# Performance work log

Measured on AMD Instinct MI355X. Metric: run time of the kernel, lower is better.

The kernel has to match this reference:

```python
import jax, jax.numpy as jnp
import numpy as np

B, N, IN_DIM, OUT_DIM = 8, 2048, 256, 256
EDGE_P = 0.02   # adjacency density
MASK_P = 0.9    # fraction of valid nodes


def setup_inputs() -> dict:
    key = jax.random.key(0)
    ks = jax.random.split(key, 8)
    x = jax.random.normal(ks[0], (B, N, IN_DIM), dtype=jnp.float32)
    adj = (jax.random.uniform(ks[1], (B, N, N)) < EDGE_P).astype(jnp.float32)
    mask = (jax.random.uniform(ks[2], (B, N)) < MASK_P).astype(jnp.float32)
    # nn.Linear(in_dim, out_dim): W [out, in], b [out]
    lim1 = 1.0 / np.sqrt(IN_DIM)
    W = jax.random.uniform(ks[3], (OUT_DIM, IN_DIM), minval=-lim1, maxval=lim1, dtype=jnp.float32)
    b = jax.random.uniform(ks[4], (OUT_DIM,), minval=-lim1, maxval=lim1, dtype=jnp.float32)
    # nn.Linear(2*out_dim, 1): weight [1, 2D] split into a1 (acts on h_i), a2 (acts on h_j)
    lim2 = 1.0 / np.sqrt(2 * OUT_DIM)
    a1 = jax.random.uniform(ks[5], (OUT_DIM,), minval=-lim2, maxval=lim2, dtype=jnp.float32)
    a2 = jax.random.uniform(ks[6], (OUT_DIM,), minval=-lim2, maxval=lim2, dtype=jnp.float32)
    att_b = jax.random.uniform(ks[7], (), minval=-lim2, maxval=lim2, dtype=jnp.float32)
    return {"x": x, "adj": adj, "mask": mask, "W": W, "b": b, "a1": a1, "a2": a2, "att_b": att_b}


def reference(x, adj, mask, W, b, a1, a2, att_b):
    # h = Linear(x): [B, N, D]
    h = jnp.einsum('bni,di->bnd', x, W) + b
    # attention(cat([h_i, h_j])) == h_i @ a1 + h_j @ a2 + att_b (linear in each half)
    s1 = h @ a1  # [B, N] -> contributes along i
    s2 = h @ a2  # [B, N] -> contributes along j
    logits = s1[:, :, None] + s2[:, None, :] + att_b  # [B, N, N]
    att = jax.nn.sigmoid(logits) * adj
    att = att * mask[:, :, None] * mask[:, None, :]
    att = att / (jnp.sum(att, axis=-1, keepdims=True) + 1e-8)
    h_new = jnp.einsum('bij,bjd->bid', att, h)
    return h_new * mask[:, :, None]
```

## Files before the change

kernel.cpp:

```cpp
#include <hip/hip_runtime.h>
#include <hip/hip_bf16.h>

#define BB 8
#define NN 2048
#define DD 256
#define MM (BB * NN)

typedef __attribute__((ext_vector_type(8))) short bf16x8_t;
typedef __attribute__((ext_vector_type(4))) float f32x4_t;

__global__ __launch_bounds__(256) void gemm_h(
    const float* __restrict__ x,
    const float* __restrict__ Wt,
    const float* __restrict__ bias,
    __hip_bfloat16* __restrict__ h)
{
    __shared__ __hip_bfloat16 As[64][72];
    __shared__ __hip_bfloat16 Bs[64][72];

    const int tid  = threadIdx.x;
    const int r    = tid >> 2;
    const int cs   = (tid & 3) * 16;
    const int w    = tid >> 6;
    const int lane = tid & 63;
    const int m16  = lane & 15;
    const int quad = lane >> 4;
    const long rowBase = (long)blockIdx.x * 64;
    const int  colBase = blockIdx.y * 64;

    f32x4_t acc[4];
#pragma unroll
    for (int c = 0; c < 4; c++) acc[c] = (f32x4_t){0.f, 0.f, 0.f, 0.f};

    for (int k0 = 0; k0 < 256; k0 += 64) {
        const float4* ag = (const float4*)(x  + (rowBase + r) * 256 + k0 + cs);
        const float4* bg = (const float4*)(Wt + (long)(colBase + r) * 256 + k0 + cs);
        float4 av[4], bv[4];
#pragma unroll
        for (int q = 0; q < 4; q++) { av[q] = ag[q]; bv[q] = bg[q]; }

        __align__(16) __hip_bfloat16 ta[16], tb[16];
#pragma unroll
        for (int q = 0; q < 4; q++) {
            ta[q * 4 + 0] = __float2bfloat16(av[q].x);
            ta[q * 4 + 1] = __float2bfloat16(av[q].y);
            ta[q * 4 + 2] = __float2bfloat16(av[q].z);
            ta[q * 4 + 3] = __float2bfloat16(av[q].w);
            tb[q * 4 + 0] = __float2bfloat16(bv[q].x);
            tb[q * 4 + 1] = __float2bfloat16(bv[q].y);
            tb[q * 4 + 2] = __float2bfloat16(bv[q].z);
            tb[q * 4 + 3] = __float2bfloat16(bv[q].w);
        }

        __syncthreads();
        *(uint4*)&As[r][cs]     = *(uint4*)&ta[0];
        *(uint4*)&As[r][cs + 8] = *(uint4*)&ta[8];
        *(uint4*)&Bs[r][cs]     = *(uint4*)&tb[0];
        *(uint4*)&Bs[r][cs + 8] = *(uint4*)&tb[8];
        __syncthreads();

#pragma unroll
        for (int kk = 0; kk < 64; kk += 32) {
            bf16x8_t af = *(const bf16x8_t*)&As[w * 16 + m16][kk + quad * 8];
#pragma unroll
            for (int c = 0; c < 4; c++) {
                bf16x8_t bf = *(const bf16x8_t*)&Bs[c * 16 + m16][kk + quad * 8];
                acc[c] = __builtin_amdgcn_mfma_f32_16x16x32_bf16(af, bf, acc[c], 0, 0, 0);
            }
        }
    }

#pragma unroll
    for (int c = 0; c < 4; c++) {
        const int col = colBase + c * 16 + m16;
        const float bv = bias[col];
#pragma unroll
        for (int reg = 0; reg < 4; reg++) {
            const long row = rowBase + w * 16 + quad * 4 + reg;
            h[row * 256 + col] = __float2bfloat16(acc[c][reg] + bv);
        }
    }
}

struct __attribute__((aligned(8))) bf4 { __hip_bfloat16 v[4]; };

__global__ __launch_bounds__(256) void s_kernel(
    const __hip_bfloat16* __restrict__ h,
    const float* __restrict__ a1,
    const float* __restrict__ a2,
    const float* __restrict__ mask,
    const float* __restrict__ attb_p,
    float* __restrict__ s1b, float* __restrict__ t2)
{
    const int w = threadIdx.x >> 6;
    const int lane = threadIdx.x & 63;
    const long row = (long)blockIdx.x * 4 + w;

    bf4 hv = *(const bf4*)(h + row * 256 + lane * 4);
    float4 A1 = *(const float4*)(a1 + lane * 4);
    float4 A2 = *(const float4*)(a2 + lane * 4);
    const float h0 = __bfloat162float(hv.v[0]), h1 = __bfloat162float(hv.v[1]);
    const float h2 = __bfloat162float(hv.v[2]), h3 = __bfloat162float(hv.v[3]);
    float p1 = h0 * A1.x + h1 * A1.y + h2 * A1.z + h3 * A1.w;
    float p2 = h0 * A2.x + h1 * A2.y + h2 * A2.z + h3 * A2.w;
#pragma unroll
    for (int off = 32; off; off >>= 1) {
        p1 += __shfl_down(p1, off);
        p2 += __shfl_down(p2, off);
    }
    if (lane == 0) {
        s1b[row] = p1 + attb_p[0];
        t2[row]  = (mask[row] != 0.f) ? p2 : -1e30f;
    }
}

__global__ __launch_bounds__(256) void attn_agg(
    const float* __restrict__ adj,
    const float* __restrict__ mask,
    const __hip_bfloat16* __restrict__ h,
    const float* __restrict__ s1b,
    const float* __restrict__ t2,
    float* __restrict__ out)
{
    __shared__ float2 s_list[1024];
    __shared__ int    s_cnt;
    __shared__ float  s_red[4];
    __shared__ float  s_inv;
    __shared__ float2 s_part[128];

    const int tid = threadIdx.x;
    const int b   = blockIdx.x & 7;
    const int i   = blockIdx.x >> 3;
    const long row   = (long)b * NN + i;
    const long mbase = (long)b * NN;

    const float mask_i = mask[row];
    if (mask_i == 0.f) {
        out[row * 256 + tid] = 0.f;
        return;
    }
    if (tid == 0) s_cnt = 0;
    __syncthreads();

    const float si = s1b[row];
    const float4* arow = (const float4*)(adj + row * NN);
    const float4* trow = (const float4*)(t2 + mbase);

    float4 A0 = arow[tid], A1 = arow[256 + tid];
    float4 T0 = trow[tid], T1 = trow[256 + tid];

    float lsum = 0.f;
#pragma unroll
    for (int g = 0; g < 2; g++) {
        const int jb = g * 1024 + tid * 4;
        const float av[4] = {g ? A1.x : A0.x, g ? A1.y : A0.y, g ? A1.z : A0.z, g ? A1.w : A0.w};
        const float tv[4] = {g ? T1.x : T0.x, g ? T1.y : T0.y, g ? T1.z : T0.z, g ? T1.w : T0.w};
#pragma unroll
        for (int e = 0; e < 4; e++) {
            const float z   = si + tv[e];
            const float sig = __builtin_amdgcn_rcpf(1.f + __expf(-z));
            const float wgt = av[e] * sig;
            lsum += wgt;
            if (wgt != 0.f) {
                const int pos = atomicAdd(&s_cnt, 1);
                if (pos < 1024)
                    s_list[pos] = make_float2(__int_as_float((jb + e) << 9), wgt);
            }
        }
    }

#pragma unroll
    for (int off = 32; off; off >>= 1) lsum += __shfl_down(lsum, off);
    const int lane = tid & 63, wv = tid >> 6;
    if (lane == 0) s_red[wv] = lsum;
    __syncthreads();
    if (tid == 0)
        s_inv = 1.f / (s_red[0] + s_red[1] + s_red[2] + s_red[3] + 1e-8f);
    __syncthreads();

    const int cnt  = min(s_cnt, 1024);
    const float inv = s_inv * mask_i;
    const char* hb = (const char*)(h + mbase * 256);
    const int g  = tid >> 7;
    const int t  = tid & 127;
    const int t4 = t * 4;
    const int half = (cnt + 1) >> 1;
    int k       = g ? half : 0;
    const int end = g ? cnt : half;

    float accx = 0.f, accy = 0.f;
    for (; k + 8 <= end; k += 8) {
        float2 e[8];
#pragma unroll
        for (int q = 0; q < 8; q++) e[q] = s_list[k + q];
        unsigned u[8];
#pragma unroll
        for (int q = 0; q < 8; q++)
            u[q] = *(const unsigned*)(hb + (__float_as_int(e[q].x) + t4));
#pragma unroll
        for (int q = 0; q < 8; q++) {
            accx += e[q].y * __uint_as_float(u[q] << 16);
            accy += e[q].y * __uint_as_float(u[q] & 0xffff0000u);
        }
    }
    for (; k + 4 <= end; k += 4) {
        float2 e[4];
#pragma unroll
        for (int q = 0; q < 4; q++) e[q] = s_list[k + q];
        unsigned u[4];
#pragma unroll
        for (int q = 0; q < 4; q++)
            u[q] = *(const unsigned*)(hb + (__float_as_int(e[q].x) + t4));
#pragma unroll
        for (int q = 0; q < 4; q++) {
            accx += e[q].y * __uint_as_float(u[q] << 16);
            accy += e[q].y * __uint_as_float(u[q] & 0xffff0000u);
        }
    }
    for (; k < end; k++) {
        float2 ee = s_list[k];
        unsigned u = *(const unsigned*)(hb + (__float_as_int(ee.x) + t4));
        accx += ee.y * __uint_as_float(u << 16);
        accy += ee.y * __uint_as_float(u & 0xffff0000u);
    }

    if (g) s_part[t] = make_float2(accx, accy);
    __syncthreads();
    if (!g) {
        const float2 p = s_part[t];
        ((float2*)(out + row * 256))[t] =
            make_float2((accx + p.x) * inv, (accy + p.y) * inv);
    }
}

extern "C" void kernel_launch(void* const* d_in, const int* in_sizes, int n_in,
                              void* d_out, int out_size, void* d_ws, size_t ws_size,
                              hipStream_t stream) {
    const float* x    = (const float*)d_in[0];
    const float* adj  = (const float*)d_in[1];
    const float* mask = (const float*)d_in[2];
    const float* W    = (const float*)d_in[3];
    const float* bias = (const float*)d_in[4];
    const float* a1   = (const float*)d_in[5];
    const float* a2   = (const float*)d_in[6];
    const float* attb = (const float*)d_in[7];
    float* out = (float*)d_out;

    __hip_bfloat16* h = (__hip_bfloat16*)d_ws;
    float* s1b = (float*)((char*)d_ws + (size_t)MM * DD * 2);
    float* t2  = s1b + MM;

    gemm_h<<<dim3(MM / 64, DD / 64), 256, 0, stream>>>(x, W, bias, h);
    s_kernel<<<MM / 4, 256, 0, stream>>>(h, a1, a2, mask, attb, s1b, t2);
    attn_agg<<<MM, 256, 0, stream>>>(adj, mask, h, s1b, t2, out);
}
```

Before: 238.5 us.

## Process one attention row per wavefront instead of one per block

The attention-aggregation kernel now gives each 64-lane wavefront its own output row, so a 256-thread block handles four rows. Each wave keeps its own shared-memory edge list, and wave shuffles replace block barriers for the sum and count reductions. Each lane now gathers four bf16 features per edge instead of two. This removes __syncthreads and cross-group partial-sum merging, and adds an exact ballot-based fallback that recomputes edges when a row has more than 512 of them. The cost is longer serial work per wave, since each wave scans 2048 adjacency entries alone.

```diff
diff --git a/kernel.cpp b/kernel.cpp
--- a/kernel.cpp
+++ b/kernel.cpp
@@ -5,6 +5,7 @@
 #define NN 2048
 #define DD 256
 #define MM (BB * NN)
+#define CAP 512
 
 typedef __attribute__((ext_vector_type(8))) short bf16x8_t;
 typedef __attribute__((ext_vector_type(4))) float f32x4_t;
@@ -114,7 +115,7 @@
     }
 }
 
-__global__ __launch_bounds__(256) void attn_agg(
+__global__ __launch_bounds__(256, 8) void attn_agg(
     const float* __restrict__ adj,
     const float* __restrict__ mask,
     const __hip_bfloat16* __restrict__ h,
@@ -122,39 +123,39 @@
     const float* __restrict__ t2,
     float* __restrict__ out)
 {
-    __shared__ float2 s_list[1024];
-    __shared__ int    s_cnt;
-    __shared__ float  s_red[4];
-    __shared__ float  s_inv;
-    __shared__ float2 s_part[128];
-
-    const int tid = threadIdx.x;
-    const int b   = blockIdx.x & 7;
-    const int i   = blockIdx.x >> 3;
+    __shared__ float2 s_list[4][CAP];
+    __shared__ int    s_cnt[4];
+
+    const int tid  = threadIdx.x;
+    const int wv   = tid >> 6;
+    const int lane = tid & 63;
+    const int b    = blockIdx.x & 7;
+    const int i    = ((blockIdx.x >> 3) << 2) + wv;
     const long row   = (long)b * NN + i;
     const long mbase = (long)b * NN;
 
+    float4* orow = (float4*)(out + row * 256);
+
     const float mask_i = mask[row];
     if (mask_i == 0.f) {
-        out[row * 256 + tid] = 0.f;
+        orow[lane] = make_float4(0.f, 0.f, 0.f, 0.f);
         return;
     }
-    if (tid == 0) s_cnt = 0;
-    __syncthreads();
+    if (lane == 0) s_cnt[wv] = 0;
 
     const float si = s1b[row];
     const float4* arow = (const float4*)(adj + row * NN);
     const float4* trow = (const float4*)(t2 + mbase);
 
-    float4 A0 = arow[tid], A1 = arow[256 + tid];
-    float4 T0 = trow[tid], T1 = trow[256 + tid];
-
     float lsum = 0.f;
-#pragma unroll
-    for (int g = 0; g < 2; g++) {
-        const int jb = g * 1024 + tid * 4;
-        const float av[4] = {g ? A1.x : A0.x, g ? A1.y : A0.y, g ? A1.z : A0.z, g ? A1.w : A0.w};
-        const float tv[4] = {g ? T1.x : T0.x, g ? T1.y : T0.y, g ? T1.z : T0.z, g ? T1.w : T0.w};
+    int   lcnt = 0;
+#pragma unroll 4
+    for (int q = 0; q < 8; q++) {
+        const float4 A = arow[q * 64 + lane];
+        const float4 T = trow[q * 64 + lane];
+        const int jb = (q * 256 + lane * 4) << 9;
+        const float av[4] = {A.x, A.y, A.z, A.w};
+        const float tv[4] = {T.x, T.y, T.z, T.w};
 #pragma unroll
         for (int e = 0; e < 4; e++) {
             const float z   = si + tv[e];
@@ -162,75 +163,81 @@
             const float wgt = av[e] * sig;
             lsum += wgt;
             if (wgt != 0.f) {
-                const int pos = atomicAdd(&s_cnt, 1);
-                if (pos < 1024)
-                    s_list[pos] = make_float2(__int_as_float((jb + e) << 9), wgt);
-            }
-        }
-    }
-
-#pragma unroll
-    for (int off = 32; off; off >>= 1) lsum += __shfl_down(lsum, off);
-    const int lane = tid & 63, wv = tid >> 6;
-    if (lane == 0) s_red[wv] = lsum;
-    __syncthreads();
-    if (tid == 0)
-        s_inv = 1.f / (s_red[0] + s_red[1] + s_red[2] + s_red[3] + 1e-8f);
-    __syncthreads();
-
-    const int cnt  = min(s_cnt, 1024);
-    const float inv = s_inv * mask_i;
-    const char* hb = (const char*)(h + mbase * 256);
-    const int g  = tid >> 7;
-    const int t  = tid & 127;
-    const int t4 = t * 4;
-    const int half = (cnt + 1) >> 1;
-    int k       = g ? half : 0;
-    const int end = g ? cnt : half;
-
-    float accx = 0.f, accy = 0.f;
-    for (; k + 8 <= end; k += 8) {
-        float2 e[8];
-#pragma unroll
-        for (int q = 0; q < 8; q++) e[q] = s_list[k + q];
-        unsigned u[8];
-#pragma unroll
-        for (int q = 0; q < 8; q++)
-            u[q] = *(const unsigned*)(hb + (__float_as_int(e[q].x) + t4));
-#pragma unroll
+                lcnt++;
+                const int pos = atomicAdd(&s_cnt[wv], 1);
+                if (pos < CAP)
+                    s_list[wv][pos] = make_float2(__int_as_float(jb + (e << 9)), wgt);
+            }
+        }
+    }
+
+#pragma unroll
+    for (int off = 32; off; off >>= 1) {
+        lsum += __shfl_down(lsum, off);
+        lcnt += __shfl_down(lcnt, off);
+    }
+    const float inv = 1.f / (__shfl(lsum, 0) + 1e-8f);
+    const int   cnt = __shfl(lcnt, 0);
+
+    const char* hb  = (const char*)(h + mbase * 256);
+    const int  loff = lane * 8;
+    float ax = 0.f, ay = 0.f, az = 0.f, aw = 0.f;
+
+    if (cnt <= CAP) {
+        const float2* lst = &s_list[wv][0];
+        int k = 0;
+        for (; k + 8 <= cnt; k += 8) {
+            float2 ee[8];
+#pragma unroll
+            for (int q = 0; q < 8; q++) ee[q] = lst[k + q];
+            uint2 u[8];
+#pragma unroll
+            for (int q = 0; q < 8; q++)
+                u[q] = *(const uint2*)(hb + __float_as_int(ee[q].x) + loff);
+#pragma unroll
+            for (int q = 0; q < 8; q++) {
+                ax += ee[q].y * __uint_as_float(u[q].x << 16);
+                ay += ee[q].y * __uint_as_float(u[q].x & 0xffff0000u);
+                az += ee[q].y * __uint_as_float(u[q].y << 16);
+                aw += ee[q].y * __uint_as_float(u[q].y & 0xffff0000u);
+            }
+        }
+        for (; k < cnt; k++) {
+            float2 ee = lst[k];
+            uint2 u = *(const uint2*)(hb + __float_as_int(ee.x) + loff);
+            ax += ee.y * __uint_as_float(u.x << 16);
+            ay += ee.y * __uint_as_float(u.x & 0xffff0000u);
+            az += ee.y * __uint_as_float(u.y << 16);
+            aw += ee.y * __uint_as_float(u.y & 0xffff0000u);
+        }
+    } else {
         for (int q = 0; q < 8; q++) {
-            accx += e[q].y * __uint_as_float(u[q] << 16);
-            accy += e[q].y * __uint_as_float(u[q] & 0xffff0000u);
-        }
-    }
-    for (; k + 4 <= end; k += 4) {
-        float2 e[4];
-#pragma unroll
-        for (int q = 0; q < 4; q++) e[q] = s_list[k + q];
-        unsigned u[4];
-#pragma unroll
-        for (int q = 0; q < 4; q++)
-            u[q] = *(const unsigned*)(hb + (__float_as_int(e[q].x) + t4));
-#pragma unroll
-        for (int q = 0; q < 4; q++) {
-            accx += e[q].y * __uint_as_float(u[q] << 16);
-            accy += e[q].y * __uint_as_float(u[q] & 0xffff0000u);
-        }
-    }
-    for (; k < end; k++) {
-        float2 ee = s_list[k];
-        unsigned u = *(const unsigned*)(hb + (__float_as_int(ee.x) + t4));
-        accx += ee.y * __uint_as_float(u << 16);
-        accy += ee.y * __uint_as_float(u & 0xffff0000u);
-    }
-
-    if (g) s_part[t] = make_float2(accx, accy);
-    __syncthreads();
-    if (!g) {
-        const float2 p = s_part[t];
-        ((float2*)(out + row * 256))[t] =
-            make_float2((accx + p.x) * inv, (accy + p.y) * inv);
-    }
+            const float4 A = arow[q * 64 + lane];
+            const float4 T = trow[q * 64 + lane];
+            const float av[4] = {A.x, A.y, A.z, A.w};
+            const float tv[4] = {T.x, T.y, T.z, T.w};
+            for (int e = 0; e < 4; e++) {
+                const float z   = si + tv[e];
+                const float sig = __builtin_amdgcn_rcpf(1.f + __expf(-z));
+                const float wgt = av[e] * sig;
+                const int   j   = q * 256 + lane * 4 + e;
+                unsigned long long bm = __ballot(wgt != 0.f);
+                while (bm) {
+                    const int s  = __ffsll((long long)bm) - 1;
+                    const float ww = __shfl(wgt, s);
+                    const int   jj = __shfl(j, s);
+                    uint2 u = *(const uint2*)(hb + (jj << 9) + loff);
+                    ax += ww * __uint_as_float(u.x << 16);
+                    ay += ww * __uint_as_float(u.x & 0xffff0000u);
+                    az += ww * __uint_as_float(u.y << 16);
+                    aw += ww * __uint_as_float(u.y & 0xffff0000u);
+                    bm &= bm - 1;
+                }
+            }
+        }
+    }
+
+    orow[lane] = make_float4(ax * inv, ay * inv, az * inv, aw * inv);
 }
 
 extern "C" void kernel_launch(void* const* d_in, const int* in_sizes, int n_in,
@@ -252,5 +259,5 @@
 
     gemm_h<<<dim3(MM / 64, DD / 64), 256, 0, stream>>>(x, W, bias, h);
     s_kernel<<<MM / 4, 256, 0, stream>>>(h, a1, a2, mask, attb, s1b, t2);
-    attn_agg<<<MM, 256, 0, stream>>>(adj, mask, h, s1b, t2, out);
-}
+    attn_agg<<<MM / 4, 256, 0, stream>>>(adj, mask, h, s1b, t2, out);
+}
```

Result: slower. 260.8 us (+9.4%).
